# Kernel tuning notes

Hardware: AMD Instinct MI355X
Metric: run time of the kernel (lower is better)

## Reference

```python
import jax, jax.numpy as jnp
import numpy as np

D_MODEL = 1024
N_HEAD = 16
D_K = D_MODEL // N_HEAD
B, S = 2, 2048


def setup_inputs() -> dict:
    key = jax.random.key(0)
    ks = jax.random.split(key, 12)
    sc = 1.0 / np.sqrt(D_MODEL)
    return {
        "q": jax.random.normal(ks[0], (B, S, D_MODEL), jnp.float32),
        "k": jax.random.normal(ks[1], (B, S, D_MODEL), jnp.float32),
        "v": jax.random.normal(ks[2], (B, S, D_MODEL), jnp.float32),
        "mask": jax.random.randint(ks[3], (B, S, S), 0, 2, jnp.int32),
        # learned params (torch Linear convention: y = x @ W + b with W pre-transposed)
        "wq": jax.random.normal(ks[4], (D_MODEL, D_MODEL), jnp.float32) * sc,
        "bq": jax.random.normal(ks[5], (D_MODEL,), jnp.float32) * sc,
        "wk": jax.random.normal(ks[6], (D_MODEL, D_MODEL), jnp.float32) * sc,  # no bias
        "wv": jax.random.normal(ks[7], (D_MODEL, D_MODEL), jnp.float32) * sc,
        "bv": jax.random.normal(ks[8], (D_MODEL,), jnp.float32) * sc,
        "wf": jax.random.normal(ks[9], (D_MODEL, D_MODEL), jnp.float32) * sc,
        "bf": jax.random.normal(ks[10], (D_MODEL,), jnp.float32) * sc,
    }


def reference(q, k, v, mask, wq, bq, wk, wv, bv, wf, bf):
    bs = q.shape[0]
    temperature = jnp.asarray(D_K ** 0.5, q.dtype)
    # projections -> [b, h, s, d_k]
    qh = (q @ wq + bq).reshape(bs, -1, N_HEAD, D_K).transpose(0, 2, 1, 3)
    kh = (k @ wk).reshape(bs, -1, N_HEAD, D_K).transpose(0, 2, 1, 3)
    vh = (v @ wv + bv).reshape(bs, -1, N_HEAD, D_K).transpose(0, 2, 1, 3)
    # scores [b, h, sq, sk]
    attn = jnp.einsum("bhqd,bhkd->bhqk", qh, kh) / temperature
    m0 = (mask[:, None, :, :] == 0)  # mask==0 -> masked out, broadcast over heads
    attn = jnp.where(m0, -jnp.inf, attn)
    attn = jax.nn.softmax(attn, axis=-1)
    attn = jnp.where(m0, 0.0, attn)
    out = jnp.einsum("bhqk,bhkd->bhqd", attn, vh)
    out = out.transpose(0, 2, 1, 3).reshape(bs, -1, D_MODEL)
    return out @ wf + bf  # dropout is identity in eval mode
```

## Files before the change

kernel.cpp:

```cpp
#include <hip/hip_runtime.h>

#define D_MODEL 1024
#define NHEAD   16
#define DK      64
#define BATCH   2
#define SEQ     2048

typedef __attribute__((ext_vector_type(8))) short bf16x8;
typedef __attribute__((ext_vector_type(4))) float f32x4;

#define QSCALE 0.18033688011f

__device__ __forceinline__ unsigned short f2b(float x) {
  unsigned u = __builtin_bit_cast(unsigned, x);
  u = (u + 0x7fffu + ((u >> 16) & 1u)) >> 16;
  return (unsigned short)u;
}
__device__ __forceinline__ unsigned short f2b_rhu(float x) {
  return (unsigned short)((__builtin_bit_cast(unsigned, x) + 0x8000u) >> 16);
}
__device__ __forceinline__ int pk2(float a, float b) {
  unsigned ua = __builtin_bit_cast(unsigned, a) + 0x8000u;
  unsigned ub = __builtin_bit_cast(unsigned, b) + 0x8000u;
  return (int)__builtin_amdgcn_perm(ub, ua, 0x07060302u);
}

typedef const __attribute__((address_space(1))) void* gas_p;
typedef __attribute__((address_space(3))) void* las_p;
__device__ __forceinline__ void gll16(const void* g, void* l) {
  __builtin_amdgcn_global_load_lds((gas_p)g, (las_p)l, 16, 0, 0);
}

__global__ __launch_bounds__(256) void cast3_kernel(
    const float* __restrict__ q, const float* __restrict__ k, const float* __restrict__ v,
    unsigned short* __restrict__ qb, unsigned short* __restrict__ kb,
    unsigned short* __restrict__ vb) {
  const float* src = blockIdx.y == 0 ? q : (blockIdx.y == 1 ? k : v);
  unsigned short* dst = blockIdx.y == 0 ? qb : (blockIdx.y == 1 ? kb : vb);
  size_t i = ((size_t)blockIdx.x * 256 + threadIdx.x) * 8;
  float4 x0 = *(const float4*)&src[i];
  float4 x1 = *(const float4*)&src[i + 4];
  int4 w;
  w.x = pk2(x0.x, x0.y); w.y = pk2(x0.z, x0.w);
  w.z = pk2(x1.x, x1.y); w.w = pk2(x1.z, x1.w);
  *(int4*)&dst[i] = w;
}

__global__ __launch_bounds__(256) void wtrans_kernel(
    const float* __restrict__ wq, const float* __restrict__ wk,
    const float* __restrict__ wv, const float* __restrict__ wf,
    unsigned short* __restrict__ wqt, unsigned short* __restrict__ wkt,
    unsigned short* __restrict__ wvt, unsigned short* __restrict__ wft) {
  __shared__ float tile[64][65];
  const float* w; unsigned short* wt;
  switch (blockIdx.z) {
    case 0: w = wq; wt = wqt; break;
    case 1: w = wk; wt = wkt; break;
    case 2: w = wv; wt = wvt; break;
    default: w = wf; wt = wft; break;
  }
  int r0 = blockIdx.y * 64, c0 = blockIdx.x * 64;
  int t = threadIdx.x;
  for (int i = 0; i < 16; ++i) {
    int idx = t + i * 256; int r = idx >> 6, c = idx & 63;
    tile[r][c] = w[(size_t)(r0 + r) * D_MODEL + c0 + c];
  }
  __syncthreads();
  for (int i = 0; i < 16; ++i) {
    int idx = t + i * 256; int r = idx >> 6, c = idx & 63;
    wt[(size_t)(c0 + r) * D_MODEL + r0 + c] = f2b(tile[c][r]);
  }
}

__global__ __launch_bounds__(256) void maskpack_kernel(
    const int* __restrict__ mask, unsigned long long* __restrict__ mbits) {
  size_t gw = ((size_t)blockIdx.x * 256 + threadIdx.x) >> 6;
  int lane = threadIdx.x & 63;
  int val = mask[gw * 64 + lane];
  unsigned long long bits = __ballot(val != 0);
  if (lane == 0) mbits[gw] = bits;
}

__global__ __launch_bounds__(256) void gemm_qkv_kernel(
    const unsigned short* __restrict__ qb, const unsigned short* __restrict__ kb,
    const unsigned short* __restrict__ vb,
    const unsigned short* __restrict__ wqt, const unsigned short* __restrict__ wkt,
    const unsigned short* __restrict__ wvt,
    const float* __restrict__ bq, const float* __restrict__ bv,
    unsigned short* __restrict__ qh, unsigned short* __restrict__ kh,
    unsigned short* __restrict__ vt) {
  __shared__ unsigned short SB[16640];
  unsigned short* As = SB;
  unsigned short* Bs = SB + 8192;
  int bid = blockIdx.x;
  int xcd = bid & 7, slot = bid >> 3;
  int mi = slot & 3, zn = slot >> 2;
  int z = zn >> 3;
  int n0 = (zn & 7) * 128;
  int m0 = (mi * 8 + xcd) * 128;
  const unsigned short* A; const unsigned short* Bt;
  switch (z) {
    case 0:  A = qb; Bt = wqt; break;
    case 1:  A = kb; Bt = wkt; break;
    default: A = vb; Bt = wvt; break;
  }
  int t = threadIdx.x, lane = t & 63, wave = t >> 6;
  int l16 = lane & 15, quad = lane >> 4;
  int wm = (wave & 1) * 64, wn = (wave >> 1) * 64;
  f32x4 zero = {0.f, 0.f, 0.f, 0.f};
  f32x4 acc[4][4];
  for (int mt = 0; mt < 4; ++mt) for (int nt = 0; nt < 4; ++nt) acc[mt][nt] = zero;

  int drow = lane >> 2, dcol = (lane & 3) * 8;
  const unsigned short* asrc = A  + (size_t)(m0 + wave * 32 + drow) * D_MODEL + dcol;
  const unsigned short* bsrc = Bt + (size_t)(n0 + wave * 32 + drow) * D_MODEL + dcol;
  unsigned short* adst = As + wave * 32 * 32 + lane * 8;
  unsigned short* bdst = Bs + wave * 32 * 32 + lane * 8;

  for (int k0 = 0; k0 < D_MODEL; k0 += 64) {
    __syncthreads();
#pragma unroll
    for (int g = 0; g < 2; ++g)
#pragma unroll
      for (int hf = 0; hf < 2; ++hf) {
        gll16(asrc + (size_t)(g * 16) * D_MODEL + k0 + hf * 32, adst + hf * 4096 + g * 512);
        gll16(bsrc + (size_t)(g * 16) * D_MODEL + k0 + hf * 32, bdst + hf * 4096 + g * 512);
      }
    __syncthreads();
#pragma unroll
    for (int half = 0; half < 2; ++half) {
      bf16x8 a[4], b[4];
      for (int mt = 0; mt < 4; ++mt)
        a[mt] = *(const bf16x8*)&As[half * 4096 + (wm + mt * 16 + l16) * 32 + quad * 8];
      for (int nt = 0; nt < 4; ++nt)
        b[nt] = *(const bf16x8*)&Bs[half * 4096 + (wn + nt * 16 + l16) * 32 + quad * 8];
      for (int mt = 0; mt < 4; ++mt)
        for (int nt = 0; nt < 4; ++nt)
          acc[mt][nt] = __builtin_amdgcn_mfma_f32_16x16x32_bf16(a[mt], b[nt], acc[mt][nt], 0, 0, 0);
    }
  }

  if (z == 2) {
    __syncthreads();
#pragma unroll
    for (int nt = 0; nt < 4; ++nt) {
      int col = wn + nt * 16 + l16;
      float bb = bv[n0 + col];
      for (int mt = 0; mt < 4; ++mt)
        for (int r = 0; r < 4; ++r)
          SB[col * 130 + wm + mt * 16 + quad * 4 + r] = f2b_rhu(acc[mt][nt][r] + bb);
    }
    __syncthreads();
    int c = t >> 1, hf = t & 1;
    int colg = n0 + c, hh = colg >> 6, dd = colg & 63;
    int b_ = m0 >> 11, sbase = m0 & (SEQ - 1);
    unsigned short* dst = vt + (((size_t)(b_ * NHEAD + hh)) * DK + dd) * SEQ + sbase + hf * 64;
#pragma unroll
    for (int j = 0; j < 8; ++j)
      *(int4*)(dst + j * 8) = *(const int4*)&SB[c * 130 + hf * 64 + j * 8];
  } else if (z == 0) {
    for (int nt = 0; nt < 4; ++nt) {
      int col = n0 + wn + nt * 16 + l16;
      float bb = bq[col];
      int h = col >> 6, d = col & 63;
      for (int mt = 0; mt < 4; ++mt)
        for (int r = 0; r < 4; ++r) {
          int row = m0 + wm + mt * 16 + quad * 4 + r;
          int b_ = row >> 11, s = row & (SEQ - 1);
          qh[(((size_t)(b_ * NHEAD + h) * SEQ) + s) * DK + d] =
              f2b_rhu((acc[mt][nt][r] + bb) * QSCALE);
        }
    }
  } else {
    for (int nt = 0; nt < 4; ++nt) {
      int col = n0 + wn + nt * 16 + l16;
      int h = col >> 6, d = col & 63;
      for (int mt = 0; mt < 4; ++mt)
        for (int r = 0; r < 4; ++r) {
          int row = m0 + wm + mt * 16 + quad * 4 + r;
          int b_ = row >> 11, s = row & (SEQ - 1);
          kh[(((size_t)(b_ * NHEAD + h) * SEQ) + s) * DK + d] = f2b_rhu(acc[mt][nt][r]);
        }
    }
  }
}

__global__ __launch_bounds__(256) void gemm_out_kernel(
    const unsigned short* __restrict__ A, const unsigned short* __restrict__ Bt,
    const float* __restrict__ bias, float* __restrict__ out) {
  __shared__ unsigned short As[64 * 64], Bs[64 * 64];
  int bid = blockIdx.x;
  int xcd = bid & 7, slot = bid >> 3;
  int mi = slot & 7, n0 = (slot >> 3) * 64;
  int m0 = (mi * 8 + xcd) * 64;
  int t = threadIdx.x, lane = t & 63, wave = t >> 6;
  int l16 = lane & 15, quad = lane >> 4;
  int wm = (wave & 1) * 32, wn = (wave >> 1) * 32;
  f32x4 zero = {0.f, 0.f, 0.f, 0.f};
  f32x4 acc[2][2];
  for (int mt = 0; mt < 2; ++mt) for (int nt = 0; nt < 2; ++nt) acc[mt][nt] = zero;

  const unsigned short* asrc = A + (size_t)(m0 + wave * 16 + (lane >> 3)) * D_MODEL + (lane & 7) * 8;
  const unsigned short* bsrc = Bt + (size_t)(n0 + wave * 16 + (lane >> 3)) * D_MODEL + (lane & 7) * 8;
  unsigned short* adst = As + wave * 16 * 64 + lane * 8;
  unsigned short* bdst = Bs + wave * 16 * 64 + lane * 8;

  for (int k0 = 0; k0 < D_MODEL; k0 += 64) {
    __syncthreads();
#pragma unroll
    for (int i = 0; i < 2; ++i) {
      gll16(asrc + k0 + (size_t)i * 8 * D_MODEL, adst + i * 512);
      gll16(bsrc + k0 + (size_t)i * 8 * D_MODEL, bdst + i * 512);
    }
    __syncthreads();
#pragma unroll
    for (int half = 0; half < 2; ++half) {
      bf16x8 a[2], b[2];
      for (int mt = 0; mt < 2; ++mt)
        a[mt] = *(const bf16x8*)&As[(wm + mt * 16 + l16) * 64 + half * 32 + quad * 8];
      for (int nt = 0; nt < 2; ++nt)
        b[nt] = *(const bf16x8*)&Bs[(wn + nt * 16 + l16) * 64 + half * 32 + quad * 8];
      for (int mt = 0; mt < 2; ++mt)
        for (int nt = 0; nt < 2; ++nt)
          acc[mt][nt] = __builtin_amdgcn_mfma_f32_16x16x32_bf16(a[mt], b[nt], acc[mt][nt], 0, 0, 0);
    }
  }
  for (int nt = 0; nt < 2; ++nt) {
    int col = n0 + wn + nt * 16 + l16;
    float bb = bias[col];
    for (int mt = 0; mt < 2; ++mt)
      for (int r = 0; r < 4; ++r) {
        int row = m0 + wm + mt * 16 + quad * 4 + r;
        out[(size_t)row * D_MODEL + col] = acc[mt][nt][r] + bb;
      }
  }
}

__global__ __launch_bounds__(256) void attn_kernel(
    const unsigned short* __restrict__ qh, const unsigned short* __restrict__ kh,
    const unsigned short* __restrict__ vt, const unsigned long long* __restrict__ mbits,
    unsigned short* __restrict__ attb) {
  __shared__ unsigned short Qs[64 * 72], Ks[64 * 72], Vs[64 * 72];
  __shared__ unsigned short Ps[4][16 * 68];
  int bid = blockIdx.x;
  int xcd = bid & 7, slot = bid >> 3;
  int bh_ = 4 * xcd + (slot >> 5);
  int qt = slot & 31;
  int b = bh_ >> 4, h = bh_ & 15;
  int t = threadIdx.x, lane = t & 63, wave = t >> 6;
  int l16 = lane & 15, quad = lane >> 4;
  size_t bh = (size_t)b * NHEAD + h;

  int sr = t >> 2, sc = (t & 3) * 8;
  const unsigned short* Qg = qh + (bh * SEQ + (size_t)qt * 64) * DK;
  *(int4*)&Qs[sr * 72 + sc]      = *(const int4*)&Qg[sr * DK + sc];
  *(int4*)&Qs[sr * 72 + sc + 32] = *(const int4*)&Qg[sr * DK + sc + 32];
  __syncthreads();
  bf16x8 qf[2];
  qf[0] = *(const bf16x8*)&Qs[(wave * 16 + l16) * 72 + quad * 8];
  qf[1] = *(const bf16x8*)&Qs[(wave * 16 + l16) * 72 + 32 + quad * 8];
  unsigned short* Pw = Ps[wave];

  const unsigned short* Kg = kh + bh * SEQ * DK;
  const unsigned short* Vg = vt + bh * DK * SEQ;
  const unsigned long long* mrow = mbits + (size_t)b * SEQ * (SEQ / 64);
  int qrow0 = qt * 64 + wave * 16 + quad * 4;

  bf16x8 ones;
#pragma unroll
  for (int i = 0; i < 8; ++i) ones[i] = (short)0x3F80;

  f32x4 zero = {0.f, 0.f, 0.f, 0.f};
  f32x4 accO[4], accRS = zero;
  for (int nt = 0; nt < 4; ++nt) accO[nt] = zero;

  for (int tk = 0; tk < SEQ / 64; ++tk) {
    __syncthreads();
    {
      const unsigned short* Kt = Kg + (size_t)tk * 64 * DK;
      *(int4*)&Ks[sr * 72 + sc]      = *(const int4*)&Kt[sr * DK + sc];
      *(int4*)&Ks[sr * 72 + sc + 32] = *(const int4*)&Kt[sr * DK + sc + 32];
      const unsigned short* Vt_ = Vg + (size_t)tk * 64;
      *(int4*)&Vs[sr * 72 + sc]      = *(const int4*)&Vt_[(size_t)sr * SEQ + sc];
      *(int4*)&Vs[sr * 72 + sc + 32] = *(const int4*)&Vt_[(size_t)sr * SEQ + sc + 32];
    }
    __syncthreads();

    unsigned long long mw[4];
#pragma unroll
    for (int r = 0; r < 4; ++r)
      mw[r] = mrow[(size_t)(qrow0 + r) * (SEQ / 64) + tk] >> l16;

    f32x4 accS[4];
    for (int nt = 0; nt < 4; ++nt) accS[nt] = zero;
#pragma unroll
    for (int step = 0; step < 2; ++step)
      for (int nt = 0; nt < 4; ++nt) {
        bf16x8 bk = *(const bf16x8*)&Ks[(nt * 16 + l16) * 72 + step * 32 + quad * 8];
        accS[nt] = __builtin_amdgcn_mfma_f32_16x16x32_bf16(qf[step], bk, accS[nt], 0, 0, 0);
      }

#pragma unroll
    for (int r = 0; r < 4; ++r) {
      unsigned lo = (unsigned)mw[r], hi = (unsigned)(mw[r] >> 32);
#pragma unroll
      for (int nt = 0; nt < 4; ++nt) {
        unsigned halfw = (nt < 2) ? lo : hi;
        const int sh = 31 - ((nt & 1) * 16);
        float pv = __builtin_amdgcn_exp2f(accS[nt][r]);
        unsigned u = (__builtin_bit_cast(unsigned, pv) + 0x8000u) >> 16;
        int mskv = ((int)(halfw << sh)) >> 31;
        Pw[(quad * 4 + r) * 68 + nt * 16 + l16] = (unsigned short)(u & (unsigned)mskv);
      }
    }

#pragma unroll
    for (int step = 0; step < 2; ++step) {
      short4 plo = *(const short4*)&Pw[l16 * 68 + step * 32 + quad * 8];
      short4 phi = *(const short4*)&Pw[l16 * 68 + step * 32 + quad * 8 + 4];
      bf16x8 ap = {plo.x, plo.y, plo.z, plo.w, phi.x, phi.y, phi.z, phi.w};
      accRS = __builtin_amdgcn_mfma_f32_16x16x32_bf16(ap, ones, accRS, 0, 0, 0);
      for (int nt = 0; nt < 4; ++nt) {
        bf16x8 bv_ = *(const bf16x8*)&Vs[(nt * 16 + l16) * 72 + step * 32 + quad * 8];
        accO[nt] = __builtin_amdgcn_mfma_f32_16x16x32_bf16(ap, bv_, accO[nt], 0, 0, 0);
      }
    }
  }

  for (int r = 0; r < 4; ++r) {
    float sden = accRS[r];
    float inv = sden > 0.f ? 1.f / sden : 0.f;
    int row = qt * 64 + wave * 16 + quad * 4 + r;
    size_t ob = ((size_t)b * SEQ + row) * D_MODEL + (size_t)h * DK;
    for (int nt = 0; nt < 4; ++nt)
      attb[ob + nt * 16 + l16] = f2b_rhu(accO[nt][r] * inv);
  }
}

extern "C" void kernel_launch(void* const* d_in, const int* in_sizes, int n_in,
                              void* d_out, int out_size, void* d_ws, size_t ws_size,
                              hipStream_t stream) {
  (void)in_sizes; (void)n_in; (void)out_size; (void)ws_size;
  const float* q    = (const float*)d_in[0];
  const float* k    = (const float*)d_in[1];
  const float* v    = (const float*)d_in[2];
  const int*   mask = (const int*)d_in[3];
  const float* wq   = (const float*)d_in[4];
  const float* bq   = (const float*)d_in[5];
  const float* wk   = (const float*)d_in[6];
  const float* wv   = (const float*)d_in[7];
  const float* bv   = (const float*)d_in[8];
  const float* wf   = (const float*)d_in[9];
  const float* bf   = (const float*)d_in[10];

  char* ws = (char*)d_ws;
  unsigned short* wft  = (unsigned short*)(ws + 0);
  unsigned short* wqt  = (unsigned short*)(ws + 2097152);
  unsigned short* wkt  = (unsigned short*)(ws + 4194304);
  unsigned short* wvt  = (unsigned short*)(ws + 6291456);
  unsigned short* attb = (unsigned short*)(ws + 2097152);
  unsigned short* qhp  = (unsigned short*)(ws + 10485760);
  unsigned short* khp  = (unsigned short*)(ws + 18874368);
  unsigned short* vtp  = (unsigned short*)(ws + 27262976);
  unsigned long long* mbits = (unsigned long long*)(ws + 35651584);
  unsigned short* vb   = (unsigned short*)(ws + 36700160);
  unsigned short* qb   = (unsigned short*)d_out;
  unsigned short* kb   = (unsigned short*)d_out + 4194304;

  hipLaunchKernelGGL(cast3_kernel, dim3(2048, 3), dim3(256), 0, stream, q, k, v, qb, kb, vb);
  hipLaunchKernelGGL(wtrans_kernel, dim3(16, 16, 4), dim3(256), 0, stream,
                     wq, wk, wv, wf, wqt, wkt, wvt, wft);
  hipLaunchKernelGGL(maskpack_kernel, dim3(32768), dim3(256), 0, stream, mask, mbits);
  hipLaunchKernelGGL(gemm_qkv_kernel, dim3(768), dim3(256), 0, stream,
                     qb, kb, vb, wqt, wkt, wvt, bq, bv, qhp, khp, vtp);
  hipLaunchKernelGGL(attn_kernel, dim3(1024), dim3(256), 0, stream,
                     qhp, khp, vtp, mbits, attb);
  hipLaunchKernelGGL(gemm_out_kernel, dim3(1024), dim3(256), 0, stream,
                     attb, wft, bf, (float*)d_out);
}
```

Measured before the change: 307.3 us.

## Use direct global-to-LDS loads with split-half layout for K/V and GEMM tiles

The attention kernel now loads K and V tiles into shared memory with gll16 direct global-to-LDS transfers instead of register round-trips. All tiles move to a layout split into two 32-column halves, giving a 64-byte row stride intended to reduce LDS bank conflicts on fragment reads. The output GEMM uses the same split layout. The P scratch buffer now reuses the Q staging area, cutting LDS use per block, which may allow more blocks per CU. The risk is that padding is removed, so bank conflicts depend on the new stride, and P writes may hit new conflicts.

Measured after the change: 300.6 us. 1.02x faster.

```diff
diff --git a/kernel.cpp b/kernel.cpp
--- a/kernel.cpp
+++ b/kernel.cpp
@@ -200,26 +200,27 @@
   f32x4 acc[2][2];
   for (int mt = 0; mt < 2; ++mt) for (int nt = 0; nt < 2; ++nt) acc[mt][nt] = zero;
 
-  const unsigned short* asrc = A + (size_t)(m0 + wave * 16 + (lane >> 3)) * D_MODEL + (lane & 7) * 8;
-  const unsigned short* bsrc = Bt + (size_t)(n0 + wave * 16 + (lane >> 3)) * D_MODEL + (lane & 7) * 8;
-  unsigned short* adst = As + wave * 16 * 64 + lane * 8;
-  unsigned short* bdst = Bs + wave * 16 * 64 + lane * 8;
+  int drow = lane >> 2, dcol = (lane & 3) * 8;
+  const unsigned short* asrc = A  + (size_t)(m0 + wave * 16 + drow) * D_MODEL + dcol;
+  const unsigned short* bsrc = Bt + (size_t)(n0 + wave * 16 + drow) * D_MODEL + dcol;
+  unsigned short* adst = As + wave * 512 + lane * 8;
+  unsigned short* bdst = Bs + wave * 512 + lane * 8;
 
   for (int k0 = 0; k0 < D_MODEL; k0 += 64) {
     __syncthreads();
 #pragma unroll
-    for (int i = 0; i < 2; ++i) {
-      gll16(asrc + k0 + (size_t)i * 8 * D_MODEL, adst + i * 512);
-      gll16(bsrc + k0 + (size_t)i * 8 * D_MODEL, bdst + i * 512);
+    for (int hf = 0; hf < 2; ++hf) {
+      gll16(asrc + k0 + hf * 32, adst + hf * 2048);
+      gll16(bsrc + k0 + hf * 32, bdst + hf * 2048);
     }
     __syncthreads();
 #pragma unroll
     for (int half = 0; half < 2; ++half) {
       bf16x8 a[2], b[2];
       for (int mt = 0; mt < 2; ++mt)
-        a[mt] = *(const bf16x8*)&As[(wm + mt * 16 + l16) * 64 + half * 32 + quad * 8];
+        a[mt] = *(const bf16x8*)&As[half * 2048 + (wm + mt * 16 + l16) * 32 + quad * 8];
       for (int nt = 0; nt < 2; ++nt)
-        b[nt] = *(const bf16x8*)&Bs[(wn + nt * 16 + l16) * 64 + half * 32 + quad * 8];
+        b[nt] = *(const bf16x8*)&Bs[half * 2048 + (wn + nt * 16 + l16) * 32 + quad * 8];
       for (int mt = 0; mt < 2; ++mt)
         for (int nt = 0; nt < 2; ++nt)
           acc[mt][nt] = __builtin_amdgcn_mfma_f32_16x16x32_bf16(a[mt], b[nt], acc[mt][nt], 0, 0, 0);
@@ -240,8 +241,8 @@
     const unsigned short* __restrict__ qh, const unsigned short* __restrict__ kh,
     const unsigned short* __restrict__ vt, const unsigned long long* __restrict__ mbits,
     unsigned short* __restrict__ attb) {
-  __shared__ unsigned short Qs[64 * 72], Ks[64 * 72], Vs[64 * 72];
-  __shared__ unsigned short Ps[4][16 * 68];
+  __shared__ unsigned short Qs[64 * 72];
+  __shared__ unsigned short Ks[64 * 64], Vs[64 * 64];
   int bid = blockIdx.x;
   int xcd = bid & 7, slot = bid >> 3;
   int bh_ = 4 * xcd + (slot >> 5);
@@ -259,13 +260,17 @@
   bf16x8 qf[2];
   qf[0] = *(const bf16x8*)&Qs[(wave * 16 + l16) * 72 + quad * 8];
   qf[1] = *(const bf16x8*)&Qs[(wave * 16 + l16) * 72 + 32 + quad * 8];
-  unsigned short* Pw = Ps[wave];
+  unsigned short* Pw = &Qs[wave * 1088];
 
   const unsigned short* Kg = kh + bh * SEQ * DK;
   const unsigned short* Vg = vt + bh * DK * SEQ;
   const unsigned long long* mrow = mbits + (size_t)b * SEQ * (SEQ / 64);
   int qrow0 = qt * 64 + wave * 16 + quad * 4;
 
+  int drow = lane >> 2, dcol = (lane & 3) * 8;
+  unsigned short* kdst = Ks + wave * 512 + lane * 8;
+  unsigned short* vdst = Vs + wave * 512 + lane * 8;
+
   bf16x8 ones;
 #pragma unroll
   for (int i = 0; i < 8; ++i) ones[i] = (short)0x3F80;
@@ -277,12 +282,13 @@
   for (int tk = 0; tk < SEQ / 64; ++tk) {
     __syncthreads();
     {
-      const unsigned short* Kt = Kg + (size_t)tk * 64 * DK;
-      *(int4*)&Ks[sr * 72 + sc]      = *(const int4*)&Kt[sr * DK + sc];
-      *(int4*)&Ks[sr * 72 + sc + 32] = *(const int4*)&Kt[sr * DK + sc + 32];
-      const unsigned short* Vt_ = Vg + (size_t)tk * 64;
-      *(int4*)&Vs[sr * 72 + sc]      = *(const int4*)&Vt_[(size_t)sr * SEQ + sc];
-      *(int4*)&Vs[sr * 72 + sc + 32] = *(const int4*)&Vt_[(size_t)sr * SEQ + sc + 32];
+      const unsigned short* Kt = Kg + ((size_t)tk * 64 + wave * 16 + drow) * DK + dcol;
+      const unsigned short* Vt_ = Vg + (size_t)(wave * 16 + drow) * SEQ + tk * 64 + dcol;
+#pragma unroll
+      for (int hf = 0; hf < 2; ++hf) {
+        gll16(Kt + hf * 32, kdst + hf * 2048);
+        gll16(Vt_ + hf * 32, vdst + hf * 2048);
+      }
     }
     __syncthreads();
 
@@ -296,7 +302,7 @@
 #pragma unroll
     for (int step = 0; step < 2; ++step)
       for (int nt = 0; nt < 4; ++nt) {
-        bf16x8 bk = *(const bf16x8*)&Ks[(nt * 16 + l16) * 72 + step * 32 + quad * 8];
+        bf16x8 bk = *(const bf16x8*)&Ks[step * 2048 + (nt * 16 + l16) * 32 + quad * 8];
         accS[nt] = __builtin_amdgcn_mfma_f32_16x16x32_bf16(qf[step], bk, accS[nt], 0, 0, 0);
       }
 
@@ -321,7 +327,7 @@
       bf16x8 ap = {plo.x, plo.y, plo.z, plo.w, phi.x, phi.y, phi.z, phi.w};
       accRS = __builtin_amdgcn_mfma_f32_16x16x32_bf16(ap, ones, accRS, 0, 0, 0);
       for (int nt = 0; nt < 4; ++nt) {
-        bf16x8 bv_ = *(const bf16x8*)&Vs[(nt * 16 + l16) * 72 + step * 32 + quad * 8];
+        bf16x8 bv_ = *(const bf16x8*)&Vs[step * 2048 + (nt * 16 + l16) * 32 + quad * 8];
         accO[nt] = __builtin_amdgcn_mfma_f32_16x16x32_bf16(ap, bv_, accO[nt], 0, 0, 0);
       }
     }
```
